# Optimization experiments

Hardware: AMD Instinct MI355X
Metric: run time of the kernel (lower is better)

The kernel has to match this reference:

```python
import jax, jax.numpy as jnp
import numpy as np

CONF_THRES = 0.25
IOU_THRES = 0.45
MAX_WH = 4096.0   # class offset for class-aware NMS (nc=1 -> offset is 0 anyway)
K = 1024          # fixed candidate pool (jit-friendly stand-in for max_nms)
MAX_DET = 300     # max detections per image (as in yolov5 NMS)


def xywh2xyxy(b):
    xy, wh = b[..., :2], b[..., 2:4]
    return jnp.concatenate([xy - wh * 0.5, xy + wh * 0.5], axis=-1)


def box_iou(a, b):
    # a: [K,4], b: [K,4] in xyxy -> [K,K] IoU
    area_a = (a[:, 2] - a[:, 0]) * (a[:, 3] - a[:, 1])
    area_b = (b[:, 2] - b[:, 0]) * (b[:, 3] - b[:, 1])
    lt = jnp.maximum(a[:, None, :2], b[None, :, :2])
    rb = jnp.minimum(a[:, None, 2:], b[None, :, 2:])
    wh = jnp.clip(rb - lt, 0.0)
    inter = wh[..., 0] * wh[..., 1]
    return inter / (area_a[:, None] + area_b[None, :] - inter + 1e-9)


def _nms_single(pred):
    # pred: [N, 6] = [xywh, obj_conf, cls_conf] (single class)
    boxes = xywh2xyxy(pred[:, :4])
    conf = pred[:, 4] * pred[:, 5]          # obj * cls  (nc=1 best-class path)
    cls = jnp.zeros_like(conf)              # single class -> class 0
    scores = jnp.where(conf > CONF_THRES, conf, -1.0)  # conf filter
    top_scores, idx = jax.lax.top_k(scores, K)          # candidates, sorted desc
    b = boxes[idx]
    c = cls[idx]
    bo = b + (c * MAX_WH)[:, None]          # class offset (no-op for nc=1)
    iou = box_iou(bo, bo)                   # [K, K]
    valid = top_scores > CONF_THRES

    def body(i, keep):
        sup = (iou[i] > IOU_THRES) & keep[i] & (jnp.arange(K) > i)
        return keep & ~sup

    keep = jax.lax.fori_loop(0, K, body, valid)  # greedy suppression
    keep_scores = jnp.where(keep, top_scores, -1.0)
    _, sel = jax.lax.top_k(keep_scores, MAX_DET)  # top MAX_DET kept, score order
    det = jnp.concatenate([b, top_scores[:, None], c[:, None]], axis=-1)[sel]
    det_valid = keep_scores[sel] > CONF_THRES
    return jnp.where(det_valid[:, None], det, 0.0)  # [MAX_DET, 6], zero-padded


def setup_inputs() -> dict:
    key = jax.random.key(0)
    k1, k2, k3, k4 = jax.random.split(key, 4)
    B, N = 32, 25200
    xy = jax.random.uniform(k1, (B, N, 2), jnp.float32) * 640.0
    wh = jax.random.uniform(k2, (B, N, 2), jnp.float32) * 160.0 + 4.0
    obj = jax.random.uniform(k3, (B, N, 1), jnp.float32)
    clsc = jax.random.uniform(k4, (B, N, 1), jnp.float32)
    x = jnp.concatenate([xy, wh, obj, clsc], axis=-1)  # [B, N, 6]
    return {"x": x}


def reference(x):
    # NMS.forward: non_max_suppression(x[0], conf_thres=0.25, iou_thres=0.45)
    return jax.vmap(_nms_single)(x)  # [B, MAX_DET, 6] (x1,y1,x2,y2,conf,cls)
```

## Files before the change

### kernel.cpp

```cpp
#include <hip/hip_runtime.h>
#include <stdint.h>

#define NBOX 25200
#define BATCH 32
#define TOPK 1024
#define MAXDET 300
#define BINCAP 2048
#define SEGCAP 512
#define NSEG 32
#define CONF_T 0.25f
#define IOU_T 0.45f
#define KEY_BIAS 0x3E800001u

#define SEGS_OFF   0u
#define SEGCNT_OFF 4194304u
#define GHIST_OFF  4198400u
#define SORTED_OFF 4460544u
#define SBOX_OFF   4722688u
#define SAREA_OFF  5246976u
#define MASKS_OFF  5378048u
#define WS_NEED    7475200u

__global__ __launch_bounds__(256) void k1_extract(const float* __restrict__ x,
                                                  unsigned long long* __restrict__ segs,
                                                  unsigned* __restrict__ segcnt,
                                                  unsigned* __restrict__ ghist) {
    const int blk = blockIdx.x;
    const int b = blk >> 3;
    const int sl = blk & 7;
    const int tid = threadIdx.x;
    const int lane = tid & 63;
    const int wv = tid >> 6;
    const int seg = sl * 4 + wv;
    const float* __restrict__ xb = x + (size_t)b * NBOX * 6;
    unsigned long long* __restrict__ sb = segs + ((size_t)b * NSEG + seg) * SEGCAP;

    __shared__ unsigned hist[256];
    hist[tid] = 0;
    __syncthreads();

    const int n0 = (seg * NBOX) / NSEG;
    const int n1 = ((seg + 1) * NBOX) / NSEG;
    unsigned base = 0;
    const unsigned long long lmask = (1ull << lane) - 1ull;
    #pragma unroll 2
    for (int n = n0 + lane; n < n1; n += 64) {
        float2 oc = *reinterpret_cast<const float2*>(xb + n * 6 + 4);
        float conf = oc.x * oc.y;
        bool take = conf > CONF_T;
        unsigned key = 0;
        if (take) {
            key = __float_as_uint(conf) - KEY_BIAS;
            atomicAdd(&hist[min(key >> 16, 255u)], 1u);
        }
        unsigned long long m = __ballot(take);
        if (take) {
            unsigned pos = base + (unsigned)__popcll(m & lmask);
            if (pos < SEGCAP)
                sb[pos] = ((unsigned long long)key << 32) | (unsigned)(~(unsigned)n);
        }
        base += (unsigned)__popcll(m);
    }
    if (lane == 0) segcnt[b * NSEG + seg] = min(base, (unsigned)SEGCAP);
    __syncthreads();
    ghist[(size_t)blk * 256 + tid] = hist[tid];
}

__global__ __launch_bounds__(1024) void k2_sort(const float* __restrict__ x,
                                                const unsigned long long* __restrict__ segs,
                                                const unsigned* __restrict__ segcnt,
                                                const unsigned* __restrict__ ghist,
                                                unsigned long long* __restrict__ sorted_g,
                                                float4* __restrict__ sbox,
                                                float* __restrict__ sarea) {
    const int b = blockIdx.x;
    const int tid = threadIdx.x;
    const int lane = tid & 63;
    const float* __restrict__ xb = x + (size_t)b * NBOX * 6;
    const unsigned long long* __restrict__ segs_b = segs + (size_t)b * NSEG * SEGCAP;

    __shared__ unsigned hist[256];
    __shared__ unsigned binstart[256];
    __shared__ unsigned bincnt[256];
    __shared__ int sh_selbin;
    __shared__ unsigned segcnt_l[NSEG];
    __shared__ unsigned long long cand[BINCAP];
    __shared__ unsigned long long sortedl[TOPK];

    if (tid < 256) {
        unsigned h = 0;
        #pragma unroll
        for (int sl = 0; sl < 8; ++sl) h += ghist[((size_t)(b * 8 + sl)) * 256 + tid];
        hist[tid] = h;
        bincnt[tid] = 0;
    }
    if (tid < NSEG) segcnt_l[tid] = segcnt[b * NSEG + tid];
    if (tid == 0) sh_selbin = 0;
    sortedl[tid] = 0ull;
    __syncthreads();

    if (tid < 64) {
        unsigned c0 = hist[tid*4+0], c1 = hist[tid*4+1];
        unsigned c2 = hist[tid*4+2], c3 = hist[tid*4+3];
        unsigned s3 = c3, s2 = c2 + s3, s1 = c1 + s2, s0 = c0 + s1;
        unsigned suf = s0;
        #pragma unroll
        for (int off = 1; off < 64; off <<= 1) {
            unsigned o = (unsigned)__shfl_down((int)suf, off);
            if (lane + off < 64) suf += o;
        }
        unsigned excl = suf - s0;
        binstart[tid*4+0] = excl + s1;
        binstart[tid*4+1] = excl + s2;
        binstart[tid*4+2] = excl + s3;
        binstart[tid*4+3] = excl;
        unsigned S0 = excl+s0, S1 = excl+s1, S2 = excl+s2, S3 = excl+s3;
        if (S0 >= TOPK && S1 < TOPK) sh_selbin = tid*4+0;
        if (S1 >= TOPK && S2 < TOPK) sh_selbin = tid*4+1;
        if (S2 >= TOPK && S3 < TOPK) sh_selbin = tid*4+2;
        if (S3 >= TOPK && excl < TOPK) sh_selbin = tid*4+3;
    }
    __syncthreads();
    const unsigned selbin = (unsigned)sh_selbin;
    const int C = (int)min(binstart[selbin] + hist[selbin], (unsigned)BINCAP);

    for (int idx = tid; idx < NSEG * SEGCAP; idx += 1024) {
        const int seg = idx >> 9;
        const int i = idx & (SEGCAP - 1);
        if (i < (int)segcnt_l[seg]) {
            unsigned long long pk = segs_b[idx];
            unsigned bin = (unsigned)(pk >> 48);
            if (bin >= selbin) {
                unsigned pos = binstart[bin] + atomicAdd(&bincnt[bin], 1u);
                if (pos < BINCAP) cand[pos] = pk;
            }
        }
    }
    __syncthreads();

    for (int e = tid; e < C; e += 1024) {
        unsigned long long mine = cand[e];
        unsigned bin = (unsigned)(mine >> 48);
        unsigned js = binstart[bin];
        unsigned je = min(js + hist[bin], (unsigned)C);
        int rank = (int)js;
        for (unsigned j = js; j < je; ++j) rank += (cand[j] > mine) ? 1 : 0;
        if (rank < TOPK) sortedl[rank] = mine;
    }
    __syncthreads();

    unsigned long long pk = sortedl[tid];
    sorted_g[(size_t)b * TOPK + tid] = pk;
    int n = (int)(~(unsigned)pk);
    if (n < 0 || n >= NBOX) n = 0;
    float2 p01 = *reinterpret_cast<const float2*>(xb + n * 6);
    float2 p23 = *reinterpret_cast<const float2*>(xb + n * 6 + 2);
    float x1 = p01.x - p23.x * 0.5f, y1 = p01.y - p23.y * 0.5f;
    float x2 = p01.x + p23.x * 0.5f, y2 = p01.y + p23.y * 0.5f;
    sbox[(size_t)b * TOPK + tid] = make_float4(x1, y1, x2, y2);
    sarea[(size_t)b * TOPK + tid] = (x2 - x1) * (y2 - y1);
}

__global__ __launch_bounds__(256) void k3_masks(const float4* __restrict__ sbox,
                                                const float* __restrict__ sarea,
                                                unsigned long long* __restrict__ masks) {
    const int b = blockIdx.y;
    const int wv = threadIdx.x >> 6;
    const int j = threadIdx.x & 63;
    const int p = blockIdx.x * 4 + wv;

    int jc = (int)((sqrtf(8.0f * (float)p + 1.0f) - 1.0f) * 0.5f);
    while ((jc + 1) * (jc + 2) / 2 <= p) ++jc;
    while (jc * (jc + 1) / 2 > p) --jc;
    const int ic = p - jc * (jc + 1) / 2;

    __shared__ float4 ibox[4][64];
    __shared__ float iar[4][64];
    ibox[wv][j] = sbox[(size_t)b * TOPK + ic * 64 + j];
    iar[wv][j]  = sarea[(size_t)b * TOPK + ic * 64 + j];
    const float4 mb = sbox[(size_t)b * TOPK + jc * 64 + j];
    const float ma  = sarea[(size_t)b * TOPK + jc * 64 + j];
    __syncthreads();

    unsigned long long w = 0ull;
    #pragma unroll 4
    for (int i = 0; i < 64; ++i) {
        float4 bi = ibox[wv][i];
        float ai = iar[wv][i];
        float xx1 = fmaxf(bi.x, mb.x);
        float yy1 = fmaxf(bi.y, mb.y);
        float xx2 = fminf(bi.z, mb.z);
        float yy2 = fminf(bi.w, mb.w);
        float iw = fmaxf(xx2 - xx1, 0.0f);
        float ih = fmaxf(yy2 - yy1, 0.0f);
        float inter = iw * ih;
        float iou = inter / (ai + ma - inter + 1e-9f);
        bool bit = (iou > IOU_T) && (ic != jc || i < j);
        if (bit) w |= (1ull << i);
    }
    masks[(((size_t)b * 16 + jc) * 16 + ic) * 64 + j] = w;
}

__global__ __launch_bounds__(1024) void k4_resolve(const unsigned long long* __restrict__ sorted_g,
                                                   const float4* __restrict__ sbox,
                                                   const unsigned long long* __restrict__ masks,
                                                   float* __restrict__ out) {
    const int b = blockIdx.x;
    const int tid = threadIdx.x;
    const int lane = tid & 63;
    const int wv = tid >> 6;

    __shared__ unsigned long long keptb[16];
    __shared__ int pre[17];
    __shared__ int sh_acc, sh_cut;

    if (tid < 16) keptb[tid] = 0ull;
    if (tid == 0) { sh_acc = 0; sh_cut = 15; }

    const unsigned long long pk = sorted_g[(size_t)b * TOPK + tid];
    bool alive = (pk != 0ull);

    unsigned long long wcs[16];
    #pragma unroll
    for (int c = 0; c < 16; ++c)
        wcs[c] = masks[(((size_t)b * 16 + wv) * 16 + c) * 64 + lane];

    #pragma unroll
    for (int c = 0; c < 16; ++c) {
        if (wv == c) {
            unsigned long long rem = __ballot(alive);
            unsigned long long kept = 0ull;
            while (rem) {
                int i = __ffsll((long long)rem) - 1;
                unsigned long long bit = 1ull << i;
                kept |= bit;
                unsigned long long row = __ballot((unsigned)((wcs[c] >> i) & 1ull));
                rem &= ~(row | bit);
            }
            alive = (kept >> lane) & 1ull;
            if (lane == 0) {
                keptb[c] = kept;
                int acc = sh_acc + (int)__popcll(kept);
                sh_acc = acc;
                if (acc >= MAXDET && c < sh_cut) sh_cut = c;
            }
        }
        __syncthreads();
        if (c >= sh_cut) break;
        if (wv > c && alive && (wcs[c] & keptb[c])) alive = false;
    }

    if (tid == 0) {
        int acc = 0;
        #pragma unroll
        for (int c = 0; c < 16; ++c) { pre[c] = acc; acc += (int)__popcll(keptb[c]); }
        pre[16] = acc;
    }
    __syncthreads();
    const int total = pre[16];

    float* __restrict__ ob = out + (size_t)b * MAXDET * 6;
    const int rank = pre[wv] + (int)__popcll(keptb[wv] & ((1ull << lane) - 1ull));
    if (alive && wv <= sh_cut && rank < MAXDET) {
        float4 bx = sbox[(size_t)b * TOPK + tid];
        float sc_ = __uint_as_float((unsigned)(pk >> 32) + KEY_BIAS);
        ob[rank * 6 + 0] = bx.x;
        ob[rank * 6 + 1] = bx.y;
        ob[rank * 6 + 2] = bx.z;
        ob[rank * 6 + 3] = bx.w;
        ob[rank * 6 + 4] = sc_;
        ob[rank * 6 + 5] = 0.0f;
    }
    for (int r = tid; r < MAXDET; r += 1024) {
        if (r >= total) {
            #pragma unroll
            for (int cc = 0; cc < 6; ++cc) ob[r * 6 + cc] = 0.0f;
        }
    }
}

__global__ __launch_bounds__(1024) void nms_single_kernel(const float* __restrict__ x,
                                                          float* __restrict__ out) {
    const int b = blockIdx.x;
    const int tid = threadIdx.x;
    const int lane = tid & 63;
    const int wv = tid >> 6;
    const float* __restrict__ xb = x + (size_t)b * NBOX * 6;

    __shared__ unsigned hist[256];
    __shared__ int sh_selbin;
    __shared__ unsigned sh_cnt;
    __shared__ unsigned long long cand[BINCAP];
    __shared__ unsigned long long keys[TOPK];
    __shared__ float4 bbox[TOPK];
    __shared__ float bar[TOPK];
    __shared__ float4 lbox[2][64];
    __shared__ float lar[2][64];
    __shared__ int listn[2];
    __shared__ int wcnt[16], wpre[16];
    __shared__ int sh_total;

    if (tid < 256) hist[tid] = 0;
    if (tid == 0) { sh_selbin = 0; sh_cnt = 0; }
    keys[tid] = 0ull;
    __syncthreads();
    for (int n = tid; n < NBOX; n += 1024) {
        float2 oc = *reinterpret_cast<const float2*>(xb + n * 6 + 4);
        float conf = oc.x * oc.y;
        if (conf > CONF_T) atomicAdd(&hist[(__float_as_uint(conf) - KEY_BIAS) >> 16], 1u);
    }
    __syncthreads();
    if (tid < 64) {
        unsigned c0 = hist[tid*4+0], c1 = hist[tid*4+1];
        unsigned c2 = hist[tid*4+2], c3 = hist[tid*4+3];
        unsigned s3 = c3, s2 = c2 + s3, s1 = c1 + s2, s0 = c0 + s1;
        unsigned suf = s0;
        #pragma unroll
        for (int off = 1; off < 64; off <<= 1) {
            unsigned o = (unsigned)__shfl_down((int)suf, off);
            if (lane + off < 64) suf += o;
        }
        unsigned excl = suf - s0;
        unsigned S0 = excl+s0, S1 = excl+s1, S2 = excl+s2, S3 = excl+s3;
        if (S0 >= TOPK && S1 < TOPK) sh_selbin = tid*4+0;
        if (S1 >= TOPK && S2 < TOPK) sh_selbin = tid*4+1;
        if (S2 >= TOPK && S3 < TOPK) sh_selbin = tid*4+2;
        if (S3 >= TOPK && excl < TOPK) sh_selbin = tid*4+3;
    }
    __syncthreads();
    const unsigned selbin = (unsigned)sh_selbin;
    for (int n = tid; n < NBOX; n += 1024) {
        float2 oc = *reinterpret_cast<const float2*>(xb + n * 6 + 4);
        float conf = oc.x * oc.y;
        bool take = false; unsigned key = 0;
        if (conf > CONF_T) {
            key = __float_as_uint(conf) - KEY_BIAS;
            take = ((key >> 16) >= selbin);
        }
        unsigned long long m = __ballot(take);
        unsigned base = 0;
        if (lane == 0 && m) base = atomicAdd(&sh_cnt, (unsigned)__popcll(m));
        base = (unsigned)__shfl((int)base, 0);
        if (take) {
            unsigned pos = base + (unsigned)__popcll(m & ((1ull << lane) - 1ull));
            if (pos < BINCAP)
                cand[pos] = ((unsigned long long)key << 32) | (unsigned)(~(unsigned)n);
        }
    }
    __syncthreads();
    const int C = (int)min(sh_cnt, (unsigned)BINCAP);
    for (int e = tid; e < C; e += 1024) {
        unsigned long long mine = cand[e];
        int rank = 0;
        #pragma unroll 8
        for (int j = 0; j < C; ++j) rank += (cand[j] > mine) ? 1 : 0;
        if (rank < TOPK) keys[rank] = mine;
    }
    __syncthreads();
    unsigned long long kk = keys[tid];
    unsigned key24 = (unsigned)(kk >> 32);
    int n = (int)(~(unsigned)kk);
    bool alive = (kk != 0ull);
    if (n < 0 || n >= NBOX) { n = 0; alive = false; }
    float sc_ = __uint_as_float(key24 + KEY_BIAS);
    float2 p01 = *reinterpret_cast<const float2*>(xb + n * 6);
    float2 p23 = *reinterpret_cast<const float2*>(xb + n * 6 + 2);
    float x1 = p01.x - p23.x * 0.5f, y1 = p01.y - p23.y * 0.5f;
    float x2 = p01.x + p23.x * 0.5f, y2 = p01.y + p23.y * 0.5f;
    float4 mybox = make_float4(x1, y1, x2, y2);
    float my_ar = (x2 - x1) * (y2 - y1);
    bbox[tid] = mybox;
    bar[tid] = my_ar;
    __syncthreads();
    const int cbase = tid & ~63;
    unsigned long long my_mask = 0ull;
    #pragma unroll 4
    for (int i = 0; i < 64; ++i) {
        float4 bi = bbox[cbase + i];
        float ai = bar[cbase + i];
        float xx1 = fmaxf(bi.x, mybox.x);
        float yy1 = fmaxf(bi.y, mybox.y);
        float xx2 = fminf(bi.z, mybox.z);
        float yy2 = fminf(bi.w, mybox.w);
        float iw = fmaxf(xx2 - xx1, 0.0f);
        float ih = fmaxf(yy2 - yy1, 0.0f);
        float inter = iw * ih;
        float iou = inter / (ai + my_ar - inter + 1e-9f);
        if (i < lane && iou > IOU_T) my_mask |= (1ull << i);
    }
    for (int c = 0; c < 16; ++c) {
        if (c > 0 && wv >= c && alive) {
            const int pb = (c - 1) & 1;
            const int m = listn[pb];
            bool sup = false;
            #pragma unroll 2
            for (int t = 0; t < m; ++t) {
                float4 bi = lbox[pb][t];
                float ai = lar[pb][t];
                float xx1 = fmaxf(bi.x, mybox.x);
                float yy1 = fmaxf(bi.y, mybox.y);
                float xx2 = fminf(bi.z, mybox.z);
                float yy2 = fminf(bi.w, mybox.w);
                float iw = fmaxf(xx2 - xx1, 0.0f);
                float ih = fmaxf(yy2 - yy1, 0.0f);
                float inter = iw * ih;
                float iou = inter / (ai + my_ar - inter + 1e-9f);
                sup = sup || (iou > IOU_T);
            }
            alive = !sup;
        }
        if (wv == c) {
            unsigned long long rem = __ballot(alive);
            unsigned long long kept = 0ull;
            while (rem) {
                int i = __ffsll((long long)rem) - 1;
                unsigned long long bit = 1ull << i;
                kept |= bit;
                unsigned long long row = __ballot((unsigned)((my_mask >> i) & 1ull));
                rem &= ~(row | bit);
            }
            alive = (kept >> lane) & 1ull;
            int nk = __popcll(kept);
            int rk = __popcll(kept & ((1ull << lane) - 1ull));
            if (alive) { lbox[c & 1][rk] = mybox; lar[c & 1][rk] = my_ar; }
            if (lane == 0) listn[c & 1] = nk;
        }
        __syncthreads();
    }
    unsigned long long m = __ballot(alive);
    if (lane == 0) wcnt[wv] = __popcll(m);
    __syncthreads();
    if (tid == 0) {
        int acc = 0;
        for (int w2 = 0; w2 < 16; ++w2) { wpre[w2] = acc; acc += wcnt[w2]; }
        sh_total = acc;
    }
    __syncthreads();
    const int rank = wpre[wv] + (int)__popcll(m & ((1ull << lane) - 1ull));
    const int total = sh_total;
    float* __restrict__ ob = out + (size_t)b * MAXDET * 6;
    if (alive && rank < MAXDET) {
        ob[rank * 6 + 0] = mybox.x;
        ob[rank * 6 + 1] = mybox.y;
        ob[rank * 6 + 2] = mybox.z;
        ob[rank * 6 + 3] = mybox.w;
        ob[rank * 6 + 4] = sc_;
        ob[rank * 6 + 5] = 0.0f;
    }
    for (int r = tid; r < MAXDET; r += 1024) {
        if (r >= total) {
            #pragma unroll
            for (int cc = 0; cc < 6; ++cc) ob[r * 6 + cc] = 0.0f;
        }
    }
}

extern "C" void kernel_launch(void* const* d_in, const int* in_sizes, int n_in,
                              void* d_out, int out_size, void* d_ws, size_t ws_size,
                              hipStream_t stream) {
    const float* x = (const float*)d_in[0];
    float* out = (float*)d_out;
    if (ws_size >= (size_t)WS_NEED) {
        char* ws = (char*)d_ws;
        unsigned long long* segs   = (unsigned long long*)(ws + SEGS_OFF);
        unsigned* segcnt           = (unsigned*)(ws + SEGCNT_OFF);
        unsigned* ghist            = (unsigned*)(ws + GHIST_OFF);
        unsigned long long* sorted = (unsigned long long*)(ws + SORTED_OFF);
        float4* sbox               = (float4*)(ws + SBOX_OFF);
        float* sarea               = (float*)(ws + SAREA_OFF);
        unsigned long long* masks  = (unsigned long long*)(ws + MASKS_OFF);
        hipLaunchKernelGGL(k1_extract, dim3(BATCH * 8), dim3(256), 0, stream,
                           x, segs, segcnt, ghist);
        hipLaunchKernelGGL(k2_sort, dim3(BATCH), dim3(1024), 0, stream,
                           x, segs, segcnt, ghist, sorted, sbox, sarea);
        hipLaunchKernelGGL(k3_masks, dim3(34, BATCH), dim3(256), 0, stream,
                           sbox, sarea, masks);
        hipLaunchKernelGGL(k4_resolve, dim3(BATCH), dim3(1024), 0, stream,
                           sorted, sbox, masks, out);
    } else {
        hipLaunchKernelGGL(nms_single_kernel, dim3(BATCH), dim3(1024), 0, stream, x, out);
    }
}
```

Before: 59.60 us.

## Drop precomputed IoU mask kernel; compute cross-chunk IoU lazily against kept boxes

Removes the k3_masks kernel that built the full 1024x1024 upper-triangular IoU bitmask. k4_resolve now builds only the in-chunk 64x64 mask itself and, for cross-chunk suppression, tests each alive box only against the boxes actually kept in earlier chunks. This saves a kernel launch and the mask traffic to and from global memory, at the cost of serial per-thread IoU loops in the resolve kernel. Separately, the extraction stage is split into 64 segments across 512 blocks instead of 32 across 256, for more parallelism in k1.

```diff
diff --git a/kernel.cpp b/kernel.cpp
--- a/kernel.cpp
+++ b/kernel.cpp
@@ -6,28 +6,38 @@
 #define TOPK 1024
 #define MAXDET 300
 #define BINCAP 2048
-#define SEGCAP 512
-#define NSEG 32
+#define SEGCAP 256
+#define NSEG 64
 #define CONF_T 0.25f
 #define IOU_T 0.45f
 #define KEY_BIAS 0x3E800001u
 
 #define SEGS_OFF   0u
 #define SEGCNT_OFF 4194304u
-#define GHIST_OFF  4198400u
-#define SORTED_OFF 4460544u
-#define SBOX_OFF   4722688u
-#define SAREA_OFF  5246976u
-#define MASKS_OFF  5378048u
-#define WS_NEED    7475200u
+#define GHIST_OFF  4202496u
+#define SORTED_OFF 4726784u
+#define SBOX_OFF   4988928u
+#define SAREA_OFF  5513216u
+#define WS_NEED    5644288u
+
+__device__ __forceinline__ float iou_of(float4 a, float ar_a, float4 bq, float ar_b) {
+    float xx1 = fmaxf(a.x, bq.x);
+    float yy1 = fmaxf(a.y, bq.y);
+    float xx2 = fminf(a.z, bq.z);
+    float yy2 = fminf(a.w, bq.w);
+    float iw = fmaxf(xx2 - xx1, 0.0f);
+    float ih = fmaxf(yy2 - yy1, 0.0f);
+    float inter = iw * ih;
+    return inter / (ar_a + ar_b - inter + 1e-9f);
+}
 
 __global__ __launch_bounds__(256) void k1_extract(const float* __restrict__ x,
                                                   unsigned long long* __restrict__ segs,
                                                   unsigned* __restrict__ segcnt,
                                                   unsigned* __restrict__ ghist) {
     const int blk = blockIdx.x;
-    const int b = blk >> 3;
-    const int sl = blk & 7;
+    const int b = blk >> 4;
+    const int sl = blk & 15;
     const int tid = threadIdx.x;
     const int lane = tid & 63;
     const int wv = tid >> 6;
@@ -90,7 +100,7 @@
     if (tid < 256) {
         unsigned h = 0;
         #pragma unroll
-        for (int sl = 0; sl < 8; ++sl) h += ghist[((size_t)(b * 8 + sl)) * 256 + tid];
+        for (int sl = 0; sl < 16; ++sl) h += ghist[((size_t)(b * 16 + sl)) * 256 + tid];
         hist[tid] = h;
         bincnt[tid] = 0;
     }
@@ -125,7 +135,7 @@
     const int C = (int)min(binstart[selbin] + hist[selbin], (unsigned)BINCAP);
 
     for (int idx = tid; idx < NSEG * SEGCAP; idx += 1024) {
-        const int seg = idx >> 9;
+        const int seg = idx >> 8;
         const int i = idx & (SEGCAP - 1);
         if (i < (int)segcnt_l[seg]) {
             unsigned long long pk = segs_b[idx];
@@ -161,55 +171,17 @@
     sarea[(size_t)b * TOPK + tid] = (x2 - x1) * (y2 - y1);
 }
 
-__global__ __launch_bounds__(256) void k3_masks(const float4* __restrict__ sbox,
-                                                const float* __restrict__ sarea,
-                                                unsigned long long* __restrict__ masks) {
-    const int b = blockIdx.y;
-    const int wv = threadIdx.x >> 6;
-    const int j = threadIdx.x & 63;
-    const int p = blockIdx.x * 4 + wv;
-
-    int jc = (int)((sqrtf(8.0f * (float)p + 1.0f) - 1.0f) * 0.5f);
-    while ((jc + 1) * (jc + 2) / 2 <= p) ++jc;
-    while (jc * (jc + 1) / 2 > p) --jc;
-    const int ic = p - jc * (jc + 1) / 2;
-
-    __shared__ float4 ibox[4][64];
-    __shared__ float iar[4][64];
-    ibox[wv][j] = sbox[(size_t)b * TOPK + ic * 64 + j];
-    iar[wv][j]  = sarea[(size_t)b * TOPK + ic * 64 + j];
-    const float4 mb = sbox[(size_t)b * TOPK + jc * 64 + j];
-    const float ma  = sarea[(size_t)b * TOPK + jc * 64 + j];
-    __syncthreads();
-
-    unsigned long long w = 0ull;
-    #pragma unroll 4
-    for (int i = 0; i < 64; ++i) {
-        float4 bi = ibox[wv][i];
-        float ai = iar[wv][i];
-        float xx1 = fmaxf(bi.x, mb.x);
-        float yy1 = fmaxf(bi.y, mb.y);
-        float xx2 = fminf(bi.z, mb.z);
-        float yy2 = fminf(bi.w, mb.w);
-        float iw = fmaxf(xx2 - xx1, 0.0f);
-        float ih = fmaxf(yy2 - yy1, 0.0f);
-        float inter = iw * ih;
-        float iou = inter / (ai + ma - inter + 1e-9f);
-        bool bit = (iou > IOU_T) && (ic != jc || i < j);
-        if (bit) w |= (1ull << i);
-    }
-    masks[(((size_t)b * 16 + jc) * 16 + ic) * 64 + j] = w;
-}
-
 __global__ __launch_bounds__(1024) void k4_resolve(const unsigned long long* __restrict__ sorted_g,
                                                    const float4* __restrict__ sbox,
-                                                   const unsigned long long* __restrict__ masks,
+                                                   const float* __restrict__ sarea,
                                                    float* __restrict__ out) {
     const int b = blockIdx.x;
     const int tid = threadIdx.x;
     const int lane = tid & 63;
     const int wv = tid >> 6;
 
+    __shared__ float4 bbox[TOPK];
+    __shared__ float bar[TOPK];
     __shared__ unsigned long long keptb[16];
     __shared__ int pre[17];
     __shared__ int sh_acc, sh_cut;
@@ -219,13 +191,20 @@
 
     const unsigned long long pk = sorted_g[(size_t)b * TOPK + tid];
     bool alive = (pk != 0ull);
-
-    unsigned long long wcs[16];
-    #pragma unroll
-    for (int c = 0; c < 16; ++c)
-        wcs[c] = masks[(((size_t)b * 16 + wv) * 16 + c) * 64 + lane];
-
-    #pragma unroll
+    const float4 mybox = sbox[(size_t)b * TOPK + tid];
+    const float my_ar = sarea[(size_t)b * TOPK + tid];
+    bbox[tid] = mybox;
+    bar[tid] = my_ar;
+    __syncthreads();
+
+    const int cbase = tid & ~63;
+    unsigned long long my_mask = 0ull;
+    #pragma unroll 4
+    for (int i = 0; i < 64; ++i) {
+        float iou = iou_of(bbox[cbase + i], bar[cbase + i], mybox, my_ar);
+        if (i < lane && iou > IOU_T) my_mask |= (1ull << i);
+    }
+
     for (int c = 0; c < 16; ++c) {
         if (wv == c) {
             unsigned long long rem = __ballot(alive);
@@ -234,7 +213,7 @@
                 int i = __ffsll((long long)rem) - 1;
                 unsigned long long bit = 1ull << i;
                 kept |= bit;
-                unsigned long long row = __ballot((unsigned)((wcs[c] >> i) & 1ull));
+                unsigned long long row = __ballot((unsigned)((my_mask >> i) & 1ull));
                 rem &= ~(row | bit);
             }
             alive = (kept >> lane) & 1ull;
@@ -247,7 +226,15 @@
         }
         __syncthreads();
         if (c >= sh_cut) break;
-        if (wv > c && alive && (wcs[c] & keptb[c])) alive = false;
+        if (wv > c && alive) {
+            unsigned long long k = keptb[c];
+            while (k) {
+                int i = __ffsll((long long)k) - 1;
+                k &= k - 1;
+                float iou = iou_of(bbox[c * 64 + i], bar[c * 64 + i], mybox, my_ar);
+                if (iou > IOU_T) { alive = false; break; }
+            }
+        }
     }
 
     if (tid == 0) {
@@ -262,12 +249,11 @@
     float* __restrict__ ob = out + (size_t)b * MAXDET * 6;
     const int rank = pre[wv] + (int)__popcll(keptb[wv] & ((1ull << lane) - 1ull));
     if (alive && wv <= sh_cut && rank < MAXDET) {
-        float4 bx = sbox[(size_t)b * TOPK + tid];
         float sc_ = __uint_as_float((unsigned)(pk >> 32) + KEY_BIAS);
-        ob[rank * 6 + 0] = bx.x;
-        ob[rank * 6 + 1] = bx.y;
-        ob[rank * 6 + 2] = bx.z;
-        ob[rank * 6 + 3] = bx.w;
+        ob[rank * 6 + 0] = mybox.x;
+        ob[rank * 6 + 1] = mybox.y;
+        ob[rank * 6 + 2] = mybox.z;
+        ob[rank * 6 + 3] = mybox.w;
         ob[rank * 6 + 4] = sc_;
         ob[rank * 6 + 5] = 0.0f;
     }
@@ -376,16 +362,7 @@
     unsigned long long my_mask = 0ull;
     #pragma unroll 4
     for (int i = 0; i < 64; ++i) {
-        float4 bi = bbox[cbase + i];
-        float ai = bar[cbase + i];
-        float xx1 = fmaxf(bi.x, mybox.x);
-        float yy1 = fmaxf(bi.y, mybox.y);
-        float xx2 = fminf(bi.z, mybox.z);
-        float yy2 = fminf(bi.w, mybox.w);
-        float iw = fmaxf(xx2 - xx1, 0.0f);
-        float ih = fmaxf(yy2 - yy1, 0.0f);
-        float inter = iw * ih;
-        float iou = inter / (ai + my_ar - inter + 1e-9f);
+        float iou = iou_of(bbox[cbase + i], bar[cbase + i], mybox, my_ar);
         if (i < lane && iou > IOU_T) my_mask |= (1ull << i);
     }
     for (int c = 0; c < 16; ++c) {
@@ -395,16 +372,7 @@
             bool sup = false;
             #pragma unroll 2
             for (int t = 0; t < m; ++t) {
-                float4 bi = lbox[pb][t];
-                float ai = lar[pb][t];
-                float xx1 = fmaxf(bi.x, mybox.x);
-                float yy1 = fmaxf(bi.y, mybox.y);
-                float xx2 = fminf(bi.z, mybox.z);
-                float yy2 = fminf(bi.w, mybox.w);
-                float iw = fmaxf(xx2 - xx1, 0.0f);
-                float ih = fmaxf(yy2 - yy1, 0.0f);
-                float inter = iw * ih;
-                float iou = inter / (ai + my_ar - inter + 1e-9f);
+                float iou = iou_of(lbox[pb][t], lar[pb][t], mybox, my_ar);
                 sup = sup || (iou > IOU_T);
             }
             alive = !sup;
@@ -468,15 +436,12 @@
         unsigned long long* sorted = (unsigned long long*)(ws + SORTED_OFF);
         float4* sbox               = (float4*)(ws + SBOX_OFF);
         float* sarea               = (float*)(ws + SAREA_OFF);
-        unsigned long long* masks  = (unsigned long long*)(ws + MASKS_OFF);
-        hipLaunchKernelGGL(k1_extract, dim3(BATCH * 8), dim3(256), 0, stream,
+        hipLaunchKernelGGL(k1_extract, dim3(512), dim3(256), 0, stream,
                            x, segs, segcnt, ghist);
         hipLaunchKernelGGL(k2_sort, dim3(BATCH), dim3(1024), 0, stream,
                            x, segs, segcnt, ghist, sorted, sbox, sarea);
-        hipLaunchKernelGGL(k3_masks, dim3(34, BATCH), dim3(256), 0, stream,
-                           sbox, sarea, masks);
         hipLaunchKernelGGL(k4_resolve, dim3(BATCH), dim3(1024), 0, stream,
-                           sorted, sbox, masks, out);
+                           sorted, sbox, sarea, out);
     } else {
         hipLaunchKernelGGL(nms_single_kernel, dim3(BATCH), dim3(1024), 0, stream, x, out);
     }
```

Result: slower. 99.11 us (+66.3%).
